# Kernel tuning notes

Hardware: AMD Instinct MI355X
Metric: run time of the kernel (lower is better)

The kernel has to match this reference:

```python
import jax, jax.numpy as jnp
import numpy as np

B, T, H, M, S, E, IN = 8, 2048, 64, 32, 20, 3, 32
EPS = 1e-8  # torch CosineSimilarity eps


def setup_inputs() -> dict:
    key = jax.random.key(0)
    ks = jax.random.split(key, 7)
    return {
        "x": jax.random.normal(ks[0], (B, T, IN), jnp.float32),
        "hidden": jax.random.normal(ks[1], (E, B, T, H), jnp.float32),
        "memory": jax.random.normal(ks[2], (S, M), jnp.float32),
        "Wq": jax.random.normal(ks[3], (E, H, M), jnp.float32),
        "Wk": jax.random.normal(ks[4], (E, H, M), jnp.float32),
        "Wv": jax.random.normal(ks[5], (E, H, M), jnp.float32),
        "input_query": jax.random.normal(ks[6], (IN, M), jnp.float32),
    }


def _cosine(a, b):
    # torch.nn.CosineSimilarity(dim=-1): each vector norm clamped to eps
    na = jnp.maximum(jnp.linalg.norm(a, axis=-1), EPS)
    nb = jnp.maximum(jnp.linalg.norm(b, axis=-1), EPS)
    return jnp.sum(a * b, axis=-1) / (na * nb)


def reference(x, hidden, memory, Wq, Wk, Wv, input_query):
    # query_mem: soft read from global memory slots
    q_in = jnp.einsum('bti,im->btm', x, input_query)           # [B,T,M]
    mem_sc = jax.nn.softmax(jnp.einsum('btm,sm->bts', q_in, memory), axis=-1)
    memories = jnp.einsum('bts,sm->btm', mem_sc, memory)       # [B,T,M]

    # per-expert tiny self-attention (vectorized over expert axis e)
    Q = jnp.einsum('ebth,ehm->ebtm', hidden, Wq)
    K = jnp.einsum('ebth,ehm->ebtm', hidden, Wk)
    V = jnp.einsum('ebth,ehm->ebtm', hidden, Wv)
    energy = jnp.einsum('ebtm,ebsm->ebts', Q, K)               # [E,B,T,T]
    att = jax.nn.softmax(energy, axis=-1)
    out = jnp.einsum('ebts,ebsm->ebtm', att, V)                # [E,B,T,M]

    cos = _cosine(memories[None], out)                         # [E,B,T]
    return jnp.moveaxis(cos, 0, -1)                            # [B,T,E]
```

## Files before the change

kernel.cpp:

```cpp
#include <hip/hip_runtime.h>
#include <hip/hip_bf16.h>

#define Bv  8
#define Tv  2048
#define Hv  64
#define Mv  32
#define Sv  20
#define Ev  3
#define INv 32
#define LOG2E 1.44269504088896340736f

typedef __attribute__((ext_vector_type(8))) _Float16 half8;
typedef __attribute__((ext_vector_type(4))) _Float16 half4v;
typedef __attribute__((ext_vector_type(2))) __fp16 fp16x2;
typedef __attribute__((ext_vector_type(4))) float float4v;

__global__ __launch_bounds__(256) void qkv_kernel(
    const float* __restrict__ hidden,
    const float* __restrict__ Wq,
    const float* __restrict__ Wk,
    const float* __restrict__ Wv,
    const float* __restrict__ x,
    const float* __restrict__ memory,
    const float* __restrict__ iq,
    _Float16* __restrict__ Qh, _Float16* __restrict__ Ql,
    _Float16* __restrict__ Kh, _Float16* __restrict__ Kl,
    _Float16* __restrict__ Vth,
    float* __restrict__ memout)
{
    __shared__ __align__(16) char sBlob[24576];
    __shared__ float sIQ[32][32];
    __shared__ float sM[20][32];

    int bid  = blockIdx.x;
    int b    = bid & 7;
    int slot = bid >> 3;
    int tile = slot & 31;
    int e    = slot >> 5;
    int tid  = threadIdx.x;
    int lane = tid & 63;
    int w    = tid >> 6;
    int quad = lane >> 4;
    int l15  = lane & 15;
    size_t eb = (size_t)(e * Bv + b);
    size_t row0 = eb * Tv + (size_t)tile * 64;
    const float* hbase = hidden + row0 * Hv;

    const float* arow = hbase + (size_t)(w * 16 + l15) * Hv + quad * 8;
    float4v a0 = __builtin_nontemporal_load((const float4v*)(arow));
    float4v a1 = __builtin_nontemporal_load((const float4v*)(arow + 4));
    float4v a2 = __builtin_nontemporal_load((const float4v*)(arow + 32));
    float4v a3 = __builtin_nontemporal_load((const float4v*)(arow + 36));

    if (e == 0) {
        for (int i = tid; i < 32 * 32; i += 256) sIQ[i >> 5][i & 31] = iq[i];
        for (int i = tid; i < 20 * 32; i += 256) sM[i >> 5][i & 31] = memory[i];
    }

    {
        const float* wsrc[3] = {Wq + (size_t)e * Hv * Mv,
                                Wk + (size_t)e * Hv * Mv,
                                Wv + (size_t)e * Hv * Mv};
        int h  = tid >> 2;
        int m0 = (tid & 3) * 8;
        int kb = h >> 3, wi = h & 7;
#pragma unroll
        for (int p = 0; p < 3; ++p) {
            const float4v* src = (const float4v*)(wsrc[p] + (size_t)tid * 8);
            float4v wa = src[0], wb = src[1];
            float wv8[8] = {wa.x, wa.y, wa.z, wa.w, wb.x, wb.y, wb.z, wb.w};
            float scale = (p == 0) ? LOG2E : 1.f;
#pragma unroll
            for (int j = 0; j < 8; ++j) {
                int c = p * 32 + m0 + j;
                float v = wv8[j] * scale;
                _Float16 hh = (_Float16)v;
                _Float16 ll = (_Float16)(v - (float)hh);
                int off = c * 128 + ((kb ^ (c & 7)) << 4) + wi * 2;
                *(_Float16*)(sBlob + off)         = hh;
                *(_Float16*)(sBlob + 12288 + off) = ll;
            }
        }
    }

    half8 aH0, aL0, aH1, aL1;
    {
        float vv[8] = {a0.x, a0.y, a0.z, a0.w, a1.x, a1.y, a1.z, a1.w};
#pragma unroll
        for (int i = 0; i < 8; ++i) {
            _Float16 hh = (_Float16)vv[i];
            aH0[i] = hh; aL0[i] = (_Float16)(vv[i] - (float)hh);
        }
        float ww[8] = {a2.x, a2.y, a2.z, a2.w, a3.x, a3.y, a3.z, a3.w};
#pragma unroll
        for (int i = 0; i < 8; ++i) {
            _Float16 hh = (_Float16)ww[i];
            aH1[i] = hh; aL1[i] = (_Float16)(ww[i] - (float)hh);
        }
    }

    __syncthreads();

    float4v accs[6];
    int x7 = l15 & 7;
#pragma unroll
    for (int ct = 0; ct < 6; ++ct) {
        const char* brow = sBlob + (ct * 16 + l15) * 128;
        half8 bH0 = *(const half8*)(brow + ((quad ^ x7) << 4));
        half8 bH1 = *(const half8*)(brow + (((4 + quad) ^ x7) << 4));
        half8 bL0 = *(const half8*)(brow + 12288 + ((quad ^ x7) << 4));
        half8 bL1 = *(const half8*)(brow + 12288 + (((4 + quad) ^ x7) << 4));
        float4v acc = {0.f, 0.f, 0.f, 0.f};
        acc = __builtin_amdgcn_mfma_f32_16x16x32_f16(aH0, bL0, acc, 0, 0, 0);
        acc = __builtin_amdgcn_mfma_f32_16x16x32_f16(aL0, bH0, acc, 0, 0, 0);
        acc = __builtin_amdgcn_mfma_f32_16x16x32_f16(aH0, bH0, acc, 0, 0, 0);
        acc = __builtin_amdgcn_mfma_f32_16x16x32_f16(aH1, bL1, acc, 0, 0, 0);
        acc = __builtin_amdgcn_mfma_f32_16x16x32_f16(aL1, bH1, acc, 0, 0, 0);
        acc = __builtin_amdgcn_mfma_f32_16x16x32_f16(aH1, bH1, acc, 0, 0, 0);
        accs[ct] = acc;
    }

    __syncthreads();

    char* sQh = sBlob;
    char* sQl = sBlob + 4096;
    char* sKh = sBlob + 8192;
    char* sKl = sBlob + 12288;
    char* sVh = sBlob + 16384;
    int rbase = w * 16 + quad * 4;
#pragma unroll
    for (int ct = 0; ct < 6; ++ct) {
        int c = ct * 16 + l15;
#pragma unroll
        for (int r = 0; r < 4; ++r) {
            int row = rbase + r;
            float v = accs[ct][r];
            if (ct < 2) {
                _Float16 h16 = (_Float16)v;
                *(_Float16*)(sQh + row * 64 + c * 2) = h16;
                *(_Float16*)(sQl + row * 64 + c * 2) = (_Float16)(v - (float)h16);
            } else if (ct < 4) {
                _Float16 h16 = (_Float16)v;
                int m = c - 32;
                int off = row * 64 + m * 2;
                *(_Float16*)(sKh + off) = h16;
                *(_Float16*)(sKl + off) = (_Float16)(v - (float)h16);
            } else {
                int d = c - 64;
                int off = d * 128 + row * 2;
                *(_Float16*)(sVh + off) = (_Float16)v;
            }
        }
    }
    __syncthreads();

    size_t pb = eb * (size_t)Tv * 32 + (size_t)tile * 2048;
    _Float16* dsts[5] = {Qh + pb, Ql + pb, Kh + pb, Kl + pb, Vth + pb};
#pragma unroll
    for (int pl = 0; pl < 5; ++pl)
        ((float4v*)dsts[pl])[tid] = ((const float4v*)(sBlob + pl * 4096))[tid];

    if (e == 0) {
        int tok4 = tid >> 2;
        int m0   = (tid & 3) * 8;
        int t = b * Tv + tile * 64 + tok4;
        const float4v* xr = (const float4v*)(x + (size_t)t * INv);
        float qm[8];
#pragma unroll
        for (int m = 0; m < 8; ++m) qm[m] = 0.f;
#pragma unroll
        for (int i4 = 0; i4 < 8; ++i4) {
            float4v xv = __builtin_nontemporal_load(&xr[i4]);
            float xs[4] = {xv.x, xv.y, xv.z, xv.w};
#pragma unroll
            for (int s = 0; s < 4; ++s) {
                int i = i4 * 4 + s;
                float xi = xs[s];
                float4v w0 = *(const float4v*)&sIQ[i][m0];
                float4v w1 = *(const float4v*)&sIQ[i][m0 + 4];
                qm[0] = fmaf(xi, w0.x, qm[0]); qm[1] = fmaf(xi, w0.y, qm[1]);
                qm[2] = fmaf(xi, w0.z, qm[2]); qm[3] = fmaf(xi, w0.w, qm[3]);
                qm[4] = fmaf(xi, w1.x, qm[4]); qm[5] = fmaf(xi, w1.y, qm[5]);
                qm[6] = fmaf(xi, w1.z, qm[6]); qm[7] = fmaf(xi, w1.w, qm[7]);
            }
        }
        float sc[20];
#pragma unroll
        for (int j = 0; j < 20; ++j) {
            float4v s0 = *(const float4v*)&sM[j][m0];
            float4v s1 = *(const float4v*)&sM[j][m0 + 4];
            float a2 = qm[0] * s0.x + qm[1] * s0.y + qm[2] * s0.z + qm[3] * s0.w
                     + qm[4] * s1.x + qm[5] * s1.y + qm[6] * s1.z + qm[7] * s1.w;
            a2 += __shfl_xor(a2, 1);
            a2 += __shfl_xor(a2, 2);
            sc[j] = a2;
        }
        float mx = sc[0];
#pragma unroll
        for (int j = 1; j < 20; ++j) mx = fmaxf(mx, sc[j]);
        float psum = 0.f, p[20];
#pragma unroll
        for (int j = 0; j < 20; ++j) { p[j] = exp2f((sc[j] - mx) * LOG2E); psum += p[j]; }
        float inv = 1.0f / psum;
        float mo[8];
#pragma unroll
        for (int m = 0; m < 8; ++m) mo[m] = 0.f;
#pragma unroll
        for (int j = 0; j < 20; ++j) {
            float pj = p[j];
            float4v s0 = *(const float4v*)&sM[j][m0];
            float4v s1 = *(const float4v*)&sM[j][m0 + 4];
            mo[0] = fmaf(pj, s0.x, mo[0]); mo[1] = fmaf(pj, s0.y, mo[1]);
            mo[2] = fmaf(pj, s0.z, mo[2]); mo[3] = fmaf(pj, s0.w, mo[3]);
            mo[4] = fmaf(pj, s1.x, mo[4]); mo[5] = fmaf(pj, s1.y, mo[5]);
            mo[6] = fmaf(pj, s1.z, mo[6]); mo[7] = fmaf(pj, s1.w, mo[7]);
        }
        float4v* outp = (float4v*)(memout + (size_t)t * Mv + m0);
        float4v o0 = {mo[0] * inv, mo[1] * inv, mo[2] * inv, mo[3] * inv};
        float4v o1 = {mo[4] * inv, mo[5] * inv, mo[6] * inv, mo[7] * inv};
        outp[0] = o0;
        outp[1] = o1;
    }
}

#define ATT_LOAD(c, KH, KL, V0, V1)                                           \
    {                                                                         \
        size_t ko = ebOff + (size_t)((c) * 64 + w * 16 + l15) * 32 + quad * 8;\
        KH = *(const half8*)(Kh + ko);                                        \
        KL = *(const half8*)(Kl + ko);                                        \
        size_t vo = ebOff + (size_t)(c) * 2048 + (size_t)l15 * 64             \
                    + w * 16 + quad * 4;                                      \
        V0 = *(const half4v*)(Vth + vo);                                      \
        V1 = *(const half4v*)(Vth + vo + 1024);                               \
    }

#define ATT_BODY(KH, KL, V0, V1)                                              \
    _Pragma("unroll")                                                         \
    for (int qt = 0; qt < 4; ++qt) {                                          \
        float4v acc = {0.f, 0.f, 0.f, 0.f};                                   \
        acc = __builtin_amdgcn_mfma_f32_16x16x32_f16(KH, qL[qt], acc, 0,0,0); \
        acc = __builtin_amdgcn_mfma_f32_16x16x32_f16(KL, qH[qt], acc, 0,0,0); \
        acc = __builtin_amdgcn_mfma_f32_16x16x32_f16(KH, qH[qt], acc, 0,0,0); \
        float pmax4 = fmaxf(fmaxf(acc[0], acc[1]), fmaxf(acc[2], acc[3]));    \
        if (!__any(pmax4 > mm[qt] - 20.0f)) continue;    \
        if (__any(pmax4 > mm[qt] + 8.0f)) {                 \
            float pm = fmaxf(pmax4, __shfl_xor(pmax4, 16));                   \
            pm = fmaxf(pm, __shfl_xor(pm, 32));                               \
            float mn = fmaxf(mm[qt], pm);                                     \
            float al = exp2f(mm[qt] - mn);                                    \
            mm[qt] = mn;                                                      \
            _Pragma("unroll")                                                 \
            for (int r = 0; r < 4; ++r) {                                     \
                O[qt][0][r] *= al; O[qt][1][r] *= al;                         \
            }                                                                 \
        }                                                                     \
        fp16x2 p01 = __builtin_amdgcn_cvt_pkrtz(exp2f(acc[0] - mm[qt]),       \
                                                exp2f(acc[1] - mm[qt]));      \
        fp16x2 p23 = __builtin_amdgcn_cvt_pkrtz(exp2f(acc[2] - mm[qt]),       \
                                                exp2f(acc[3] - mm[qt]));      \
        unsigned long long up =                                               \
            ((unsigned long long)__builtin_bit_cast(unsigned int, p23) << 32) \
            | __builtin_bit_cast(unsigned int, p01);                          \
        half4v pB = __builtin_bit_cast(half4v, up);                           \
        O[qt][0] = __builtin_amdgcn_mfma_f32_16x16x16f16(V0, pB, O[qt][0],    \
                                                         0, 0, 0);            \
        O[qt][1] = __builtin_amdgcn_mfma_f32_16x16x16f16(V1, pB, O[qt][1],    \
                                                         0, 0, 0);            \
    }

__global__ __launch_bounds__(256, 3) void attn_kernel(
    const _Float16* __restrict__ Qh, const _Float16* __restrict__ Ql,
    const _Float16* __restrict__ Kh, const _Float16* __restrict__ Kl,
    const _Float16* __restrict__ Vth,
    const float* __restrict__ memv,
    float* __restrict__ out)
{
    __shared__ float sO[4][64][33];
    __shared__ float sMw[4][64];

    int bid  = blockIdx.x;
    int xcd  = bid & 7;
    int slot = bid >> 3;
    int tile = slot & 31;
    int ebi  = xcd + ((slot >> 5) << 3);
    int e    = ebi >> 3;
    int b    = ebi & 7;
    int tid  = threadIdx.x;
    int lane = tid & 63;
    int w    = tid >> 6;
    int quad = lane >> 4;
    int l15  = lane & 15;
    size_t eb = (size_t)ebi;
    size_t ebOff = eb * (size_t)Tv * 32;

    half8 qH[4], qL[4];
#pragma unroll
    for (int qt = 0; qt < 4; ++qt) {
        size_t qoff = ebOff + (size_t)(tile * 64 + qt * 16 + l15) * 32 + quad * 8;
        qH[qt] = *(const half8*)(Qh + qoff);
        qL[qt] = *(const half8*)(Ql + qoff);
    }

    float4v O[4][2];
#pragma unroll
    for (int qt = 0; qt < 4; ++qt) {
        O[qt][0] = {0.f, 0.f, 0.f, 0.f};
        O[qt][1] = {0.f, 0.f, 0.f, 0.f};
    }
    float mm[4] = {-3.0e38f, -3.0e38f, -3.0e38f, -3.0e38f};

    half8 kHa, kLa, kHb, kLb;
    half4v v0a, v1a, v0b, v1b;
    ATT_LOAD(0, kHa, kLa, v0a, v1a);

    for (int c = 0; c < 32; c += 2) {
        ATT_LOAD(c + 1, kHb, kLb, v0b, v1b);
        ATT_BODY(kHa, kLa, v0a, v1a);
        if (c + 2 < 32) ATT_LOAD(c + 2, kHa, kLa, v0a, v1a);
        ATT_BODY(kHb, kLb, v0b, v1b);
    }

#pragma unroll
    for (int qt = 0; qt < 4; ++qt) {
        int q = qt * 16 + l15;
        sMw[w][q] = mm[qt];
#pragma unroll
        for (int dh = 0; dh < 2; ++dh)
#pragma unroll
            for (int r = 0; r < 4; ++r)
                sO[w][q][dh * 16 + quad * 4 + r] = O[qt][dh][r];
    }
    __syncthreads();

    int q  = tid >> 2;
    int dq = tid & 3;
    float ms0 = sMw[0][q], ms1 = sMw[1][q], ms2 = sMw[2][q], ms3 = sMw[3][q];
    float M  = fmaxf(fmaxf(ms0, ms1), fmaxf(ms2, ms3));
    float g0 = exp2f(ms0 - M), g1 = exp2f(ms1 - M);
    float g2 = exp2f(ms2 - M), g3 = exp2f(ms3 - M);
    const float* mb = memv + ((size_t)b * Tv + tile * 64 + q) * 32 + dq * 8;
    float dotm = 0.f, oo = 0.f, mm2 = 0.f;
#pragma unroll
    for (int j = 0; j < 8; ++j) {
        int d = dq * 8 + j;
        float o = g0 * sO[0][q][d] + g1 * sO[1][q][d]
                + g2 * sO[2][q][d] + g3 * sO[3][q][d];
        float mvv = mb[j];
        dotm = fmaf(o, mvv, dotm);
        oo   = fmaf(o, o, oo);
        mm2  = fmaf(mvv, mvv, mm2);
    }
    dotm += __shfl_xor(dotm, 1); dotm += __shfl_xor(dotm, 2);
    oo   += __shfl_xor(oo, 1);   oo   += __shfl_xor(oo, 2);
    mm2  += __shfl_xor(mm2, 1);  mm2  += __shfl_xor(mm2, 2);
    if (dq == 0) {
        float na = fmaxf(sqrtf(mm2), 1e-8f);
        float nb = fmaxf(sqrtf(oo), 1e-30f);
        out[((size_t)b * Tv + tile * 64 + q) * Ev + e] = dotm / (na * nb);
    }
}

extern "C" void kernel_launch(void* const* d_in, const int* in_sizes, int n_in,
                              void* d_out, int out_size, void* d_ws, size_t ws_size,
                              hipStream_t stream) {
    const float* x      = (const float*)d_in[0];
    const float* hidden = (const float*)d_in[1];
    const float* memory = (const float*)d_in[2];
    const float* Wq     = (const float*)d_in[3];
    const float* Wk     = (const float*)d_in[4];
    const float* Wv     = (const float*)d_in[5];
    const float* iq     = (const float*)d_in[6];
    float* out          = (float*)d_out;

    char* ws = (char*)d_ws;
    const size_t PLANE = (size_t)Ev * Bv * Tv * 32 * 2;
    float*    memout = (float*)ws;
    _Float16* Qh  = (_Float16*)(ws + 2097152);
    _Float16* Ql  = (_Float16*)(ws + 2097152 + PLANE);
    _Float16* Kh  = (_Float16*)(ws + 2097152 + 2 * PLANE);
    _Float16* Kl  = (_Float16*)(ws + 2097152 + 3 * PLANE);
    _Float16* Vth = (_Float16*)(ws + 2097152 + 4 * PLANE);

    qkv_kernel<<<Ev * Bv * (Tv / 64), 256, 0, stream>>>(hidden, Wq, Wk, Wv,
                                                        x, memory, iq,
                                                        Qh, Ql, Kh, Kl, Vth, memout);
    attn_kernel<<<Ev * Bv * (Tv / 64), 256, 0, stream>>>(Qh, Ql, Kh, Kl, Vth,
                                                         memout, out);
}
```

Baseline: 134.3 us.

## Fuse QKV projection and attention into one persistent kernel with grid barrier

Merges the projection kernel and the attention kernel into a single launch of 768 blocks. A global atomic counter acts as a grid-wide barrier, reset by a tiny init kernel. Q stays in shared memory instead of being written to and reread from global memory, so only K, V and the memory readout go through the workspace. This removes one kernel launch gap and the Q round trip, but requires all 768 blocks to be co-resident (launch bound of 3 blocks per CU). If they are not, the barrier deadlocks until the guard counter expires, and it adds a second small launch plus spin-wait overhead.

```diff
diff --git a/kernel.cpp b/kernel.cpp
--- a/kernel.cpp
+++ b/kernel.cpp
@@ -9,219 +9,15 @@
 #define Ev  3
 #define INv 32
 #define LOG2E 1.44269504088896340736f
+#define NBLK 768u
 
 typedef __attribute__((ext_vector_type(8))) _Float16 half8;
 typedef __attribute__((ext_vector_type(4))) _Float16 half4v;
 typedef __attribute__((ext_vector_type(2))) __fp16 fp16x2;
 typedef __attribute__((ext_vector_type(4))) float float4v;
 
-__global__ __launch_bounds__(256) void qkv_kernel(
-    const float* __restrict__ hidden,
-    const float* __restrict__ Wq,
-    const float* __restrict__ Wk,
-    const float* __restrict__ Wv,
-    const float* __restrict__ x,
-    const float* __restrict__ memory,
-    const float* __restrict__ iq,
-    _Float16* __restrict__ Qh, _Float16* __restrict__ Ql,
-    _Float16* __restrict__ Kh, _Float16* __restrict__ Kl,
-    _Float16* __restrict__ Vth,
-    float* __restrict__ memout)
-{
-    __shared__ __align__(16) char sBlob[24576];
-    __shared__ float sIQ[32][32];
-    __shared__ float sM[20][32];
-
-    int bid  = blockIdx.x;
-    int b    = bid & 7;
-    int slot = bid >> 3;
-    int tile = slot & 31;
-    int e    = slot >> 5;
-    int tid  = threadIdx.x;
-    int lane = tid & 63;
-    int w    = tid >> 6;
-    int quad = lane >> 4;
-    int l15  = lane & 15;
-    size_t eb = (size_t)(e * Bv + b);
-    size_t row0 = eb * Tv + (size_t)tile * 64;
-    const float* hbase = hidden + row0 * Hv;
-
-    const float* arow = hbase + (size_t)(w * 16 + l15) * Hv + quad * 8;
-    float4v a0 = __builtin_nontemporal_load((const float4v*)(arow));
-    float4v a1 = __builtin_nontemporal_load((const float4v*)(arow + 4));
-    float4v a2 = __builtin_nontemporal_load((const float4v*)(arow + 32));
-    float4v a3 = __builtin_nontemporal_load((const float4v*)(arow + 36));
-
-    if (e == 0) {
-        for (int i = tid; i < 32 * 32; i += 256) sIQ[i >> 5][i & 31] = iq[i];
-        for (int i = tid; i < 20 * 32; i += 256) sM[i >> 5][i & 31] = memory[i];
-    }
-
-    {
-        const float* wsrc[3] = {Wq + (size_t)e * Hv * Mv,
-                                Wk + (size_t)e * Hv * Mv,
-                                Wv + (size_t)e * Hv * Mv};
-        int h  = tid >> 2;
-        int m0 = (tid & 3) * 8;
-        int kb = h >> 3, wi = h & 7;
-#pragma unroll
-        for (int p = 0; p < 3; ++p) {
-            const float4v* src = (const float4v*)(wsrc[p] + (size_t)tid * 8);
-            float4v wa = src[0], wb = src[1];
-            float wv8[8] = {wa.x, wa.y, wa.z, wa.w, wb.x, wb.y, wb.z, wb.w};
-            float scale = (p == 0) ? LOG2E : 1.f;
-#pragma unroll
-            for (int j = 0; j < 8; ++j) {
-                int c = p * 32 + m0 + j;
-                float v = wv8[j] * scale;
-                _Float16 hh = (_Float16)v;
-                _Float16 ll = (_Float16)(v - (float)hh);
-                int off = c * 128 + ((kb ^ (c & 7)) << 4) + wi * 2;
-                *(_Float16*)(sBlob + off)         = hh;
-                *(_Float16*)(sBlob + 12288 + off) = ll;
-            }
-        }
-    }
-
-    half8 aH0, aL0, aH1, aL1;
-    {
-        float vv[8] = {a0.x, a0.y, a0.z, a0.w, a1.x, a1.y, a1.z, a1.w};
-#pragma unroll
-        for (int i = 0; i < 8; ++i) {
-            _Float16 hh = (_Float16)vv[i];
-            aH0[i] = hh; aL0[i] = (_Float16)(vv[i] - (float)hh);
-        }
-        float ww[8] = {a2.x, a2.y, a2.z, a2.w, a3.x, a3.y, a3.z, a3.w};
-#pragma unroll
-        for (int i = 0; i < 8; ++i) {
-            _Float16 hh = (_Float16)ww[i];
-            aH1[i] = hh; aL1[i] = (_Float16)(ww[i] - (float)hh);
-        }
-    }
-
-    __syncthreads();
-
-    float4v accs[6];
-    int x7 = l15 & 7;
-#pragma unroll
-    for (int ct = 0; ct < 6; ++ct) {
-        const char* brow = sBlob + (ct * 16 + l15) * 128;
-        half8 bH0 = *(const half8*)(brow + ((quad ^ x7) << 4));
-        half8 bH1 = *(const half8*)(brow + (((4 + quad) ^ x7) << 4));
-        half8 bL0 = *(const half8*)(brow + 12288 + ((quad ^ x7) << 4));
-        half8 bL1 = *(const half8*)(brow + 12288 + (((4 + quad) ^ x7) << 4));
-        float4v acc = {0.f, 0.f, 0.f, 0.f};
-        acc = __builtin_amdgcn_mfma_f32_16x16x32_f16(aH0, bL0, acc, 0, 0, 0);
-        acc = __builtin_amdgcn_mfma_f32_16x16x32_f16(aL0, bH0, acc, 0, 0, 0);
-        acc = __builtin_amdgcn_mfma_f32_16x16x32_f16(aH0, bH0, acc, 0, 0, 0);
-        acc = __builtin_amdgcn_mfma_f32_16x16x32_f16(aH1, bL1, acc, 0, 0, 0);
-        acc = __builtin_amdgcn_mfma_f32_16x16x32_f16(aL1, bH1, acc, 0, 0, 0);
-        acc = __builtin_amdgcn_mfma_f32_16x16x32_f16(aH1, bH1, acc, 0, 0, 0);
-        accs[ct] = acc;
-    }
-
-    __syncthreads();
-
-    char* sQh = sBlob;
-    char* sQl = sBlob + 4096;
-    char* sKh = sBlob + 8192;
-    char* sKl = sBlob + 12288;
-    char* sVh = sBlob + 16384;
-    int rbase = w * 16 + quad * 4;
-#pragma unroll
-    for (int ct = 0; ct < 6; ++ct) {
-        int c = ct * 16 + l15;
-#pragma unroll
-        for (int r = 0; r < 4; ++r) {
-            int row = rbase + r;
-            float v = accs[ct][r];
-            if (ct < 2) {
-                _Float16 h16 = (_Float16)v;
-                *(_Float16*)(sQh + row * 64 + c * 2) = h16;
-                *(_Float16*)(sQl + row * 64 + c * 2) = (_Float16)(v - (float)h16);
-            } else if (ct < 4) {
-                _Float16 h16 = (_Float16)v;
-                int m = c - 32;
-                int off = row * 64 + m * 2;
-                *(_Float16*)(sKh + off) = h16;
-                *(_Float16*)(sKl + off) = (_Float16)(v - (float)h16);
-            } else {
-                int d = c - 64;
-                int off = d * 128 + row * 2;
-                *(_Float16*)(sVh + off) = (_Float16)v;
-            }
-        }
-    }
-    __syncthreads();
-
-    size_t pb = eb * (size_t)Tv * 32 + (size_t)tile * 2048;
-    _Float16* dsts[5] = {Qh + pb, Ql + pb, Kh + pb, Kl + pb, Vth + pb};
-#pragma unroll
-    for (int pl = 0; pl < 5; ++pl)
-        ((float4v*)dsts[pl])[tid] = ((const float4v*)(sBlob + pl * 4096))[tid];
-
-    if (e == 0) {
-        int tok4 = tid >> 2;
-        int m0   = (tid & 3) * 8;
-        int t = b * Tv + tile * 64 + tok4;
-        const float4v* xr = (const float4v*)(x + (size_t)t * INv);
-        float qm[8];
-#pragma unroll
-        for (int m = 0; m < 8; ++m) qm[m] = 0.f;
-#pragma unroll
-        for (int i4 = 0; i4 < 8; ++i4) {
-            float4v xv = __builtin_nontemporal_load(&xr[i4]);
-            float xs[4] = {xv.x, xv.y, xv.z, xv.w};
-#pragma unroll
-            for (int s = 0; s < 4; ++s) {
-                int i = i4 * 4 + s;
-                float xi = xs[s];
-                float4v w0 = *(const float4v*)&sIQ[i][m0];
-                float4v w1 = *(const float4v*)&sIQ[i][m0 + 4];
-                qm[0] = fmaf(xi, w0.x, qm[0]); qm[1] = fmaf(xi, w0.y, qm[1]);
-                qm[2] = fmaf(xi, w0.z, qm[2]); qm[3] = fmaf(xi, w0.w, qm[3]);
-                qm[4] = fmaf(xi, w1.x, qm[4]); qm[5] = fmaf(xi, w1.y, qm[5]);
-                qm[6] = fmaf(xi, w1.z, qm[6]); qm[7] = fmaf(xi, w1.w, qm[7]);
-            }
-        }
-        float sc[20];
-#pragma unroll
-        for (int j = 0; j < 20; ++j) {
-            float4v s0 = *(const float4v*)&sM[j][m0];
-            float4v s1 = *(const float4v*)&sM[j][m0 + 4];
-            float a2 = qm[0] * s0.x + qm[1] * s0.y + qm[2] * s0.z + qm[3] * s0.w
-                     + qm[4] * s1.x + qm[5] * s1.y + qm[6] * s1.z + qm[7] * s1.w;
-            a2 += __shfl_xor(a2, 1);
-            a2 += __shfl_xor(a2, 2);
-            sc[j] = a2;
-        }
-        float mx = sc[0];
-#pragma unroll
-        for (int j = 1; j < 20; ++j) mx = fmaxf(mx, sc[j]);
-        float psum = 0.f, p[20];
-#pragma unroll
-        for (int j = 0; j < 20; ++j) { p[j] = exp2f((sc[j] - mx) * LOG2E); psum += p[j]; }
-        float inv = 1.0f / psum;
-        float mo[8];
-#pragma unroll
-        for (int m = 0; m < 8; ++m) mo[m] = 0.f;
-#pragma unroll
-        for (int j = 0; j < 20; ++j) {
-            float pj = p[j];
-            float4v s0 = *(const float4v*)&sM[j][m0];
-            float4v s1 = *(const float4v*)&sM[j][m0 + 4];
-            mo[0] = fmaf(pj, s0.x, mo[0]); mo[1] = fmaf(pj, s0.y, mo[1]);
-            mo[2] = fmaf(pj, s0.z, mo[2]); mo[3] = fmaf(pj, s0.w, mo[3]);
-            mo[4] = fmaf(pj, s1.x, mo[4]); mo[5] = fmaf(pj, s1.y, mo[5]);
-            mo[6] = fmaf(pj, s1.z, mo[6]); mo[7] = fmaf(pj, s1.w, mo[7]);
-        }
-        float4v* outp = (float4v*)(memout + (size_t)t * Mv + m0);
-        float4v o0 = {mo[0] * inv, mo[1] * inv, mo[2] * inv, mo[3] * inv};
-        float4v o1 = {mo[4] * inv, mo[5] * inv, mo[6] * inv, mo[7] * inv};
-        outp[0] = o0;
-        outp[1] = o1;
-    }
-}
+
+__global__ void init_bar(unsigned int* c) { *c = 0u; }
 
 #define ATT_LOAD(c, KH, KL, V0, V1)                                           \
     {                                                                         \
@@ -268,95 +64,310 @@
                                                          0, 0, 0);            \
     }
 
-__global__ __launch_bounds__(256, 3) void attn_kernel(
-    const _Float16* __restrict__ Qh, const _Float16* __restrict__ Ql,
-    const _Float16* __restrict__ Kh, const _Float16* __restrict__ Kl,
-    const _Float16* __restrict__ Vth,
-    const float* __restrict__ memv,
-    float* __restrict__ out)
+__global__ __launch_bounds__(256, 3) void fused_kernel(
+    const float* __restrict__ hidden,
+    const float* __restrict__ Wq,
+    const float* __restrict__ Wk,
+    const float* __restrict__ Wv,
+    const float* __restrict__ x,
+    const float* __restrict__ memory,
+    const float* __restrict__ iq,
+    _Float16* __restrict__ Kh, _Float16* __restrict__ Kl,
+    _Float16* __restrict__ Vth,
+    float* __restrict__ memout,
+    float* __restrict__ out,
+    unsigned int* __restrict__ bar)
 {
-    __shared__ float sO[4][64][33];
-    __shared__ float sMw[4][64];
+    __shared__ __align__(16) char arena[34816];
 
     int bid  = blockIdx.x;
-    int xcd  = bid & 7;
-    int slot = bid >> 3;
-    int tile = slot & 31;
-    int ebi  = xcd + ((slot >> 5) << 3);
-    int e    = ebi >> 3;
-    int b    = ebi & 7;
     int tid  = threadIdx.x;
     int lane = tid & 63;
     int w    = tid >> 6;
     int quad = lane >> 4;
     int l15  = lane & 15;
-    size_t eb = (size_t)ebi;
-    size_t ebOff = eb * (size_t)Tv * 32;
-
-    half8 qH[4], qL[4];
-#pragma unroll
-    for (int qt = 0; qt < 4; ++qt) {
-        size_t qoff = ebOff + (size_t)(tile * 64 + qt * 16 + l15) * 32 + quad * 8;
-        qH[qt] = *(const half8*)(Qh + qoff);
-        qL[qt] = *(const half8*)(Ql + qoff);
-    }
-
-    float4v O[4][2];
-#pragma unroll
-    for (int qt = 0; qt < 4; ++qt) {
-        O[qt][0] = {0.f, 0.f, 0.f, 0.f};
-        O[qt][1] = {0.f, 0.f, 0.f, 0.f};
-    }
-    float mm[4] = {-3.0e38f, -3.0e38f, -3.0e38f, -3.0e38f};
-
-    half8 kHa, kLa, kHb, kLb;
-    half4v v0a, v1a, v0b, v1b;
-    ATT_LOAD(0, kHa, kLa, v0a, v1a);
-
-    for (int c = 0; c < 32; c += 2) {
-        ATT_LOAD(c + 1, kHb, kLb, v0b, v1b);
-        ATT_BODY(kHa, kLa, v0a, v1a);
-        if (c + 2 < 32) ATT_LOAD(c + 2, kHa, kLa, v0a, v1a);
-        ATT_BODY(kHb, kLb, v0b, v1b);
-    }
-
-#pragma unroll
-    for (int qt = 0; qt < 4; ++qt) {
-        int q = qt * 16 + l15;
-        sMw[w][q] = mm[qt];
-#pragma unroll
-        for (int dh = 0; dh < 2; ++dh)
-#pragma unroll
-            for (int r = 0; r < 4; ++r)
-                sO[w][q][dh * 16 + quad * 4 + r] = O[qt][dh][r];
-    }
+
+    int b    = bid & 7;
+    int slot = bid >> 3;
+    int tile = slot & 31;
+    int e    = slot >> 5;
+    size_t eb = (size_t)(e * Bv + b);
+
+    {
+        char* sBlob = arena;
+        float (*sIQ)[32] = (float (*)[32])(arena + 24576);
+        float (*sM)[32]  = (float (*)[32])(arena + 28672);
+
+        size_t row0 = eb * Tv + (size_t)tile * 64;
+        const float* hbase = hidden + row0 * Hv;
+
+        const float* arow = hbase + (size_t)(w * 16 + l15) * Hv + quad * 8;
+        float4v a0 = __builtin_nontemporal_load((const float4v*)(arow));
+        float4v a1 = __builtin_nontemporal_load((const float4v*)(arow + 4));
+        float4v a2 = __builtin_nontemporal_load((const float4v*)(arow + 32));
+        float4v a3 = __builtin_nontemporal_load((const float4v*)(arow + 36));
+
+        if (e == 0) {
+            for (int i = tid; i < 32 * 32; i += 256) sIQ[i >> 5][i & 31] = iq[i];
+            for (int i = tid; i < 20 * 32; i += 256) sM[i >> 5][i & 31] = memory[i];
+        }
+
+        {
+            const float* wsrc[3] = {Wq + (size_t)e * Hv * Mv,
+                                    Wk + (size_t)e * Hv * Mv,
+                                    Wv + (size_t)e * Hv * Mv};
+            int m0 = (tid & 3) * 8;
+            int h  = tid >> 2;
+            int kb = h >> 3, wi = h & 7;
+#pragma unroll
+            for (int p = 0; p < 3; ++p) {
+                const float4v* src = (const float4v*)(wsrc[p] + (size_t)tid * 8);
+                float4v wa = src[0], wb = src[1];
+                float wv8[8] = {wa.x, wa.y, wa.z, wa.w, wb.x, wb.y, wb.z, wb.w};
+                float scale = (p == 0) ? LOG2E : 1.f;
+#pragma unroll
+                for (int j = 0; j < 8; ++j) {
+                    int c = p * 32 + m0 + j;
+                    float v = wv8[j] * scale;
+                    _Float16 hh = (_Float16)v;
+                    _Float16 ll = (_Float16)(v - (float)hh);
+                    int off = c * 128 + ((kb ^ (c & 7)) << 4) + wi * 2;
+                    *(_Float16*)(sBlob + off)         = hh;
+                    *(_Float16*)(sBlob + 12288 + off) = ll;
+                }
+            }
+        }
+
+        half8 aH0, aL0, aH1, aL1;
+        {
+            float vv[8] = {a0.x, a0.y, a0.z, a0.w, a1.x, a1.y, a1.z, a1.w};
+#pragma unroll
+            for (int i = 0; i < 8; ++i) {
+                _Float16 hh = (_Float16)vv[i];
+                aH0[i] = hh; aL0[i] = (_Float16)(vv[i] - (float)hh);
+            }
+            float ww[8] = {a2.x, a2.y, a2.z, a2.w, a3.x, a3.y, a3.z, a3.w};
+#pragma unroll
+            for (int i = 0; i < 8; ++i) {
+                _Float16 hh = (_Float16)ww[i];
+                aH1[i] = hh; aL1[i] = (_Float16)(ww[i] - (float)hh);
+            }
+        }
+
+        __syncthreads();
+
+        float4v accs[6];
+        int x7 = l15 & 7;
+#pragma unroll
+        for (int ct = 0; ct < 6; ++ct) {
+            const char* brow = sBlob + (ct * 16 + l15) * 128;
+            half8 bH0 = *(const half8*)(brow + ((quad ^ x7) << 4));
+            half8 bH1 = *(const half8*)(brow + (((4 + quad) ^ x7) << 4));
+            half8 bL0 = *(const half8*)(brow + 12288 + ((quad ^ x7) << 4));
+            half8 bL1 = *(const half8*)(brow + 12288 + (((4 + quad) ^ x7) << 4));
+            float4v acc = {0.f, 0.f, 0.f, 0.f};
+            acc = __builtin_amdgcn_mfma_f32_16x16x32_f16(aH0, bL0, acc, 0, 0, 0);
+            acc = __builtin_amdgcn_mfma_f32_16x16x32_f16(aL0, bH0, acc, 0, 0, 0);
+            acc = __builtin_amdgcn_mfma_f32_16x16x32_f16(aH0, bH0, acc, 0, 0, 0);
+            acc = __builtin_amdgcn_mfma_f32_16x16x32_f16(aH1, bL1, acc, 0, 0, 0);
+            acc = __builtin_amdgcn_mfma_f32_16x16x32_f16(aL1, bH1, acc, 0, 0, 0);
+            acc = __builtin_amdgcn_mfma_f32_16x16x32_f16(aH1, bH1, acc, 0, 0, 0);
+            accs[ct] = acc;
+        }
+
+        __syncthreads();
+
+        char* sQh = sBlob;
+        char* sQl = sBlob + 4096;
+        char* sKh = sBlob + 8192;
+        char* sKl = sBlob + 12288;
+        char* sVh = sBlob + 16384;
+        int rbase = w * 16 + quad * 4;
+#pragma unroll
+        for (int ct = 0; ct < 6; ++ct) {
+            int c = ct * 16 + l15;
+#pragma unroll
+            for (int r = 0; r < 4; ++r) {
+                int row = rbase + r;
+                float v = accs[ct][r];
+                if (ct < 2) {
+                    _Float16 h16 = (_Float16)v;
+                    *(_Float16*)(sQh + row * 64 + c * 2) = h16;
+                    *(_Float16*)(sQl + row * 64 + c * 2) = (_Float16)(v - (float)h16);
+                } else if (ct < 4) {
+                    _Float16 h16 = (_Float16)v;
+                    int m = c - 32;
+                    int off = row * 64 + m * 2;
+                    *(_Float16*)(sKh + off) = h16;
+                    *(_Float16*)(sKl + off) = (_Float16)(v - (float)h16);
+                } else {
+                    int d = c - 64;
+                    int off = d * 128 + row * 2;
+                    *(_Float16*)(sVh + off) = (_Float16)v;
+                }
+            }
+        }
+        __syncthreads();
+
+        size_t pb = eb * (size_t)Tv * 32 + (size_t)tile * 2048;
+        _Float16* dsts[3] = {Kh + pb, Kl + pb, Vth + pb};
+#pragma unroll
+        for (int pl = 0; pl < 3; ++pl)
+            ((float4v*)dsts[pl])[tid] = ((const float4v*)(sBlob + (pl + 2) * 4096))[tid];
+
+        if (e == 0) {
+            int tok4 = tid >> 2;
+            int m0   = (tid & 3) * 8;
+            int t = b * Tv + tile * 64 + tok4;
+            const float4v* xr = (const float4v*)(x + (size_t)t * INv);
+            float qm[8];
+#pragma unroll
+            for (int m = 0; m < 8; ++m) qm[m] = 0.f;
+#pragma unroll
+            for (int i4 = 0; i4 < 8; ++i4) {
+                float4v xv = __builtin_nontemporal_load(&xr[i4]);
+                float xs[4] = {xv.x, xv.y, xv.z, xv.w};
+#pragma unroll
+                for (int s = 0; s < 4; ++s) {
+                    int i = i4 * 4 + s;
+                    float xi = xs[s];
+                    float4v w0 = *(const float4v*)&sIQ[i][m0];
+                    float4v w1 = *(const float4v*)&sIQ[i][m0 + 4];
+                    qm[0] = fmaf(xi, w0.x, qm[0]); qm[1] = fmaf(xi, w0.y, qm[1]);
+                    qm[2] = fmaf(xi, w0.z, qm[2]); qm[3] = fmaf(xi, w0.w, qm[3]);
+                    qm[4] = fmaf(xi, w1.x, qm[4]); qm[5] = fmaf(xi, w1.y, qm[5]);
+                    qm[6] = fmaf(xi, w1.z, qm[6]); qm[7] = fmaf(xi, w1.w, qm[7]);
+                }
+            }
+            float sc[20];
+#pragma unroll
+            for (int j = 0; j < 20; ++j) {
+                float4v s0 = *(const float4v*)&sM[j][m0];
+                float4v s1 = *(const float4v*)&sM[j][m0 + 4];
+                float a2 = qm[0]*s0.x + qm[1]*s0.y + qm[2]*s0.z + qm[3]*s0.w
+                         + qm[4]*s1.x + qm[5]*s1.y + qm[6]*s1.z + qm[7]*s1.w;
+                a2 += __shfl_xor(a2, 1);
+                a2 += __shfl_xor(a2, 2);
+                sc[j] = a2;
+            }
+            float mx = sc[0];
+#pragma unroll
+            for (int j = 1; j < 20; ++j) mx = fmaxf(mx, sc[j]);
+            float psum = 0.f, p[20];
+#pragma unroll
+            for (int j = 0; j < 20; ++j) { p[j] = exp2f((sc[j] - mx) * LOG2E); psum += p[j]; }
+            float inv = 1.0f / psum;
+            float mo[8];
+#pragma unroll
+            for (int m = 0; m < 8; ++m) mo[m] = 0.f;
+#pragma unroll
+            for (int j = 0; j < 20; ++j) {
+                float pj = p[j];
+                float4v s0 = *(const float4v*)&sM[j][m0];
+                float4v s1 = *(const float4v*)&sM[j][m0 + 4];
+                mo[0] = fmaf(pj, s0.x, mo[0]); mo[1] = fmaf(pj, s0.y, mo[1]);
+                mo[2] = fmaf(pj, s0.z, mo[2]); mo[3] = fmaf(pj, s0.w, mo[3]);
+                mo[4] = fmaf(pj, s1.x, mo[4]); mo[5] = fmaf(pj, s1.y, mo[5]);
+                mo[6] = fmaf(pj, s1.z, mo[6]); mo[7] = fmaf(pj, s1.w, mo[7]);
+            }
+            float4v* outp = (float4v*)(memout + (size_t)t * Mv + m0);
+            float4v o0 = {mo[0]*inv, mo[1]*inv, mo[2]*inv, mo[3]*inv};
+            float4v o1 = {mo[4]*inv, mo[5]*inv, mo[6]*inv, mo[7]*inv};
+            outp[0] = o0;
+            outp[1] = o1;
+        }
+    }
+
     __syncthreads();
-
-    int q  = tid >> 2;
-    int dq = tid & 3;
-    float ms0 = sMw[0][q], ms1 = sMw[1][q], ms2 = sMw[2][q], ms3 = sMw[3][q];
-    float M  = fmaxf(fmaxf(ms0, ms1), fmaxf(ms2, ms3));
-    float g0 = exp2f(ms0 - M), g1 = exp2f(ms1 - M);
-    float g2 = exp2f(ms2 - M), g3 = exp2f(ms3 - M);
-    const float* mb = memv + ((size_t)b * Tv + tile * 64 + q) * 32 + dq * 8;
-    float dotm = 0.f, oo = 0.f, mm2 = 0.f;
-#pragma unroll
-    for (int j = 0; j < 8; ++j) {
-        int d = dq * 8 + j;
-        float o = g0 * sO[0][q][d] + g1 * sO[1][q][d]
-                + g2 * sO[2][q][d] + g3 * sO[3][q][d];
-        float mvv = mb[j];
-        dotm = fmaf(o, mvv, dotm);
-        oo   = fmaf(o, o, oo);
-        mm2  = fmaf(mvv, mvv, mm2);
-    }
-    dotm += __shfl_xor(dotm, 1); dotm += __shfl_xor(dotm, 2);
-    oo   += __shfl_xor(oo, 1);   oo   += __shfl_xor(oo, 2);
-    mm2  += __shfl_xor(mm2, 1);  mm2  += __shfl_xor(mm2, 2);
-    if (dq == 0) {
-        float na = fmaxf(sqrtf(mm2), 1e-8f);
-        float nb = fmaxf(sqrtf(oo), 1e-30f);
-        out[((size_t)b * Tv + tile * 64 + q) * Ev + e] = dotm / (na * nb);
+    if (tid == 0) {
+        __threadfence();
+        __hip_atomic_fetch_add(bar, 1u, __ATOMIC_ACQ_REL, __HIP_MEMORY_SCOPE_AGENT);
+        int guard = 0;
+        while (__hip_atomic_load(bar, __ATOMIC_ACQUIRE, __HIP_MEMORY_SCOPE_AGENT)
+                   < NBLK && guard < 100000000) {
+            __builtin_amdgcn_s_sleep(16);
+            ++guard;
+        }
+    }
+    __syncthreads();
+    __threadfence();
+
+    {
+        size_t ebOff = eb * (size_t)Tv * 32;
+
+        half8 qH[4], qL[4];
+        {
+            const char* sQh = arena;
+            const char* sQl = arena + 4096;
+#pragma unroll
+            for (int qt = 0; qt < 4; ++qt) {
+                int off = (qt * 16 + l15) * 64 + quad * 16;
+                qH[qt] = *(const half8*)(sQh + off);
+                qL[qt] = *(const half8*)(sQl + off);
+            }
+        }
+        __syncthreads();
+
+        float (*sO)[64][33] = (float (*)[64][33])arena;
+        float (*sMw)[64]    = (float (*)[64])(arena + 33792);
+
+        float4v O[4][2];
+#pragma unroll
+        for (int qt = 0; qt < 4; ++qt) {
+            O[qt][0] = {0.f, 0.f, 0.f, 0.f};
+            O[qt][1] = {0.f, 0.f, 0.f, 0.f};
+        }
+        float mm[4] = {-3.0e38f, -3.0e38f, -3.0e38f, -3.0e38f};
+
+        half8 kHa, kLa, kHb, kLb;
+        half4v v0a, v1a, v0b, v1b;
+        ATT_LOAD(0, kHa, kLa, v0a, v1a);
+
+        for (int c = 0; c < 32; c += 2) {
+            ATT_LOAD(c + 1, kHb, kLb, v0b, v1b);
+            ATT_BODY(kHa, kLa, v0a, v1a);
+            if (c + 2 < 32) ATT_LOAD(c + 2, kHa, kLa, v0a, v1a);
+            ATT_BODY(kHb, kLb, v0b, v1b);
+        }
+
+#pragma unroll
+        for (int qt = 0; qt < 4; ++qt) {
+            int q = qt * 16 + l15;
+            sMw[w][q] = mm[qt];
+#pragma unroll
+            for (int dh = 0; dh < 2; ++dh)
+#pragma unroll
+                for (int r = 0; r < 4; ++r)
+                    sO[w][q][dh * 16 + quad * 4 + r] = O[qt][dh][r];
+        }
+        __syncthreads();
+
+        int q  = tid >> 2;
+        int dq = tid & 3;
+        float ms0 = sMw[0][q], ms1 = sMw[1][q], ms2 = sMw[2][q], ms3 = sMw[3][q];
+        float M  = fmaxf(fmaxf(ms0, ms1), fmaxf(ms2, ms3));
+        float g0 = exp2f(ms0 - M), g1 = exp2f(ms1 - M);
+        float g2 = exp2f(ms2 - M), g3 = exp2f(ms3 - M);
+        const float* mb = memout + ((size_t)b * Tv + tile * 64 + q) * 32 + dq * 8;
+        float dotm = 0.f, oo = 0.f, mm2 = 0.f;
+#pragma unroll
+        for (int j = 0; j < 8; ++j) {
+            int d = dq * 8 + j;
+            float o = g0 * sO[0][q][d] + g1 * sO[1][q][d]
+                    + g2 * sO[2][q][d] + g3 * sO[3][q][d];
+            float mvv = mb[j];
+            dotm = fmaf(o, mvv, dotm);
+            oo   = fmaf(o, o, oo);
+            mm2  = fmaf(mvv, mvv, mm2);
+        }
+        dotm += __shfl_xor(dotm, 1); dotm += __shfl_xor(dotm, 2);
+        oo   += __shfl_xor(oo, 1);   oo   += __shfl_xor(oo, 2);
+        mm2  += __shfl_xor(mm2, 1);  mm2  += __shfl_xor(mm2, 2);
+        if (dq == 0) {
+            float na = fmaxf(sqrtf(mm2), 1e-8f);
+            float nb = fmaxf(sqrtf(oo), 1e-30f);
+            out[((size_t)b * Tv + tile * 64 + q) * Ev + e] = dotm / (na * nb);
+        }
     }
 }
 
@@ -374,16 +385,14 @@
 
     char* ws = (char*)d_ws;
     const size_t PLANE = (size_t)Ev * Bv * Tv * 32 * 2;
-    float*    memout = (float*)ws;
-    _Float16* Qh  = (_Float16*)(ws + 2097152);
-    _Float16* Ql  = (_Float16*)(ws + 2097152 + PLANE);
+    float*        memout = (float*)ws;
+    unsigned int* bar    = (unsigned int*)(ws + 2097152);
     _Float16* Kh  = (_Float16*)(ws + 2097152 + 2 * PLANE);
     _Float16* Kl  = (_Float16*)(ws + 2097152 + 3 * PLANE);
     _Float16* Vth = (_Float16*)(ws + 2097152 + 4 * PLANE);
 
-    qkv_kernel<<<Ev * Bv * (Tv / 64), 256, 0, stream>>>(hidden, Wq, Wk, Wv,
-                                                        x, memory, iq,
-                                                        Qh, Ql, Kh, Kl, Vth, memout);
-    attn_kernel<<<Ev * Bv * (Tv / 64), 256, 0, stream>>>(Qh, Ql, Kh, Kl, Vth,
-                                                         memout, out);
+    init_bar<<<1, 1, 0, stream>>>(bar);
+    fused_kernel<<<Ev * Bv * (Tv / 64), 256, 0, stream>>>(
+        hidden, Wq, Wk, Wv, x, memory, iq,
+        Kh, Kl, Vth, memout, out, bar);
 }
```

New measurement: 285.1 us. 2.12x slower.
